# Optimization experiments

Hardware: AMD Instinct MI355X
Metric: run time of the kernel (lower is better)

Reference implementation:

```python
import jax, jax.numpy as jnp
import numpy as np

D = 1024
H = 16
DH = D // H
SCALE = DH ** -0.5
EPS = 1e-5


def setup_inputs() -> dict:
    key = jax.random.key(0)
    ks = jax.random.split(key, 8)
    B, K = 256, 64
    hidden = jax.random.normal(ks[0], (B, K, D), dtype=jnp.float32)
    active_mask = jax.random.bernoulli(ks[1], 0.5, (B, K))
    w = lambda k: jax.random.normal(k, (D, D), dtype=jnp.float32) * 0.02
    return {
        "hidden": hidden,
        "active_mask": active_mask,
        "W_q": w(ks[2]),
        "W_k": w(ks[3]),
        "W_v": w(ks[4]),
        "W_o": w(ks[5]),
        "ln_gamma": jnp.ones((D,), dtype=jnp.float32),
        "ln_beta": jnp.zeros((D,), dtype=jnp.float32),
    }


def reference(hidden, active_mask, W_q, W_k, W_v, W_o, ln_gamma, ln_beta):
    B, K, _ = hidden.shape
    # Linear (no bias): x @ W.T, then split heads -> [B, H, K, Dh]
    def heads(t):
        return t.reshape(B, K, H, DH).transpose(0, 2, 1, 3)
    Q = heads(hidden @ W_q.T)
    Km = heads(hidden @ W_k.T)
    V = heads(hidden @ W_v.T)
    # scaled dot-product scores [B, H, K, K]
    attn = jnp.einsum("bhqd,bhkd->bhqk", Q, Km) * SCALE
    attn = jax.nn.softmax(attn, axis=-1)
    # post-softmax row masking: inactive query rows get zero attention
    row_mask = active_mask[:, None, :, None].astype(attn.dtype)  # [B,1,K,1]
    attn = attn * row_mask
    out = jnp.einsum("bhqk,bhkd->bhqd", attn, V)
    out = out.transpose(0, 2, 1, 3).reshape(B, K, D)
    out = out @ W_o.T
    # gated residual: residual attention output only on active modules
    active_f = active_mask[:, :, None].astype(hidden.dtype)
    h_final = hidden + active_f * out
    # LayerNorm over last dim
    mu = jnp.mean(h_final, axis=-1, keepdims=True)
    var = jnp.var(h_final, axis=-1, keepdims=True)
    h_norm = (h_final - mu) * jax.lax.rsqrt(var + EPS)
    return h_norm * ln_gamma + ln_beta
```

## Files before the change

kernel.cpp:

```cpp
#include <hip/hip_runtime.h>
#include <hip/hip_bf16.h>
#include <stdint.h>

#define D_DIM 1024
#define NH 16
#define DHD 64
#define SEQ 64
#define NBATCH 256
#define M_TOT 16384
#define ATT_SCALE 0.125f
#define LN_EPS 1e-5f

#define BM 256
#define BN 256
#define BKT 64
#define NTK (D_DIM / BKT)

typedef __attribute__((ext_vector_type(8))) short bf16x8;
typedef __attribute__((ext_vector_type(4))) float f32x4;

__device__ __forceinline__ float bf2f(short s) {
  union { uint32_t u; float f; } c;
  c.u = ((uint32_t)(uint16_t)s) << 16;
  return c.f;
}

__device__ __forceinline__ short f2bf(float f) {
  union { __hip_bfloat16 h; short s; } c; c.h = __float2bfloat16(f);
  return c.s;
}

__device__ __forceinline__ bf16x8 cvt8(float4 a, float4 b) {
  bf16x8 r;
  r[0] = f2bf(a.x); r[1] = f2bf(a.y); r[2] = f2bf(a.z); r[3] = f2bf(a.w);
  r[4] = f2bf(b.x); r[5] = f2bf(b.y); r[6] = f2bf(b.z); r[7] = f2bf(b.w);
  return r;
}

__device__ __forceinline__ void cp16(const void* g, void* l) {
  __builtin_amdgcn_global_load_lds(
      (const __attribute__((address_space(1))) uint32_t*)g,
      (__attribute__((address_space(3))) uint32_t*)l, 16, 0, 0);
}

__global__ void conv_all(const float* __restrict__ Wq, const float* __restrict__ Wk,
                         const float* __restrict__ Wv, const float* __restrict__ Wo,
                         const float* __restrict__ H,
                         __hip_bfloat16* __restrict__ Wall,
                         __hip_bfloat16* __restrict__ Hb) {
  const size_t idx8 = ((size_t)blockIdx.x * 256 + threadIdx.x) * 8;
  const size_t WE = (size_t)4 * D_DIM * D_DIM;
  const float* src;
  __hip_bfloat16* dst;
  if (idx8 < WE) {
    int z = (int)(idx8 >> 20);
    size_t off = idx8 & ((1u << 20) - 1);
    src = ((z == 0) ? Wq : (z == 1) ? Wk : (z == 2) ? Wv : Wo) + off;
    dst = Wall + idx8;
  } else {
    size_t off = idx8 - WE;
    src = H + off;
    dst = Hb + off;
  }
  float4 a = ((const float4*)src)[0];
  float4 b = ((const float4*)src)[1];
  *(bf16x8*)(short*)dst = cvt8(a, b);
}

#define GEMM_TILE(J, CUR, NXT) do {                                           \
                 \
    _Pragma("unroll") for (int i_ = 0; i_ < 4; ++i_) {                        \
      af[i_][0] = *(const bf16x8*)(LdsA[CUR] + aoff + i_ * 2048 + colsw0);    \
      af[i_][1] = *(const bf16x8*)(LdsA[CUR] + aoff + i_ * 2048 + colsw1);    \
    }                                                                         \
    _Pragma("unroll") for (int q_ = 0; q_ < 2; ++q_) {                        \
      bfr[q_][0] = *(const bf16x8*)(LdsB[CUR] + boff + q_ * 2048 + colsw0);   \
      bfr[q_][1] = *(const bf16x8*)(LdsB[CUR] + boff + q_ * 2048 + colsw1);   \
    }                                                                         \
    __builtin_amdgcn_s_barrier();                                             \
    __asm volatile("s_waitcnt lgkmcnt(0)" ::: "memory");                      \
    __builtin_amdgcn_s_setprio(1);                                            \
    _Pragma("unroll") for (int i_ = 0; i_ < 4; ++i_)                          \
      _Pragma("unroll") for (int q_ = 0; q_ < 2; ++q_) {                      \
        acc[i_][q_] = __builtin_amdgcn_mfma_f32_16x16x32_bf16(                \
            af[i_][0], bfr[q_][0], acc[i_][q_], 0, 0, 0);                     \
        acc[i_][q_] = __builtin_amdgcn_mfma_f32_16x16x32_bf16(                \
            af[i_][1], bfr[q_][1], acc[i_][q_], 0, 0, 0);                     \
      }                                                                       \
    __builtin_amdgcn_s_setprio(0);                                            \
    __builtin_amdgcn_s_barrier();                                             \
           \
    _Pragma("unroll") for (int q_ = 0; q_ < 2; ++q_) {                        \
      bfr[2 + q_][0] =                                                        \
          *(const bf16x8*)(LdsB[CUR] + boff + (2 + q_) * 2048 + colsw0);      \
      bfr[2 + q_][1] =                                                        \
          *(const bf16x8*)(LdsB[CUR] + boff + (2 + q_) * 2048 + colsw1);      \
    }                                                                         \
    if ((J) + 2 < NTK) { STG_A(CUR, (J) + 2, 0); STG_A(CUR, (J) + 2, 2); }    \
    __builtin_amdgcn_s_barrier();                                             \
    __asm volatile("s_waitcnt lgkmcnt(0)" ::: "memory");                      \
    __builtin_amdgcn_s_setprio(1);                                            \
    _Pragma("unroll") for (int i_ = 0; i_ < 4; ++i_)                          \
      _Pragma("unroll") for (int q_ = 0; q_ < 2; ++q_) {                      \
        acc[i_][2 + q_] = __builtin_amdgcn_mfma_f32_16x16x32_bf16(            \
            af[i_][0], bfr[2 + q_][0], acc[i_][2 + q_], 0, 0, 0);             \
        acc[i_][2 + q_] = __builtin_amdgcn_mfma_f32_16x16x32_bf16(            \
            af[i_][1], bfr[2 + q_][1], acc[i_][2 + q_], 0, 0, 0);             \
      }                                                                       \
    __builtin_amdgcn_s_setprio(0);                                            \
    __builtin_amdgcn_s_barrier();                                             \
            \
    _Pragma("unroll") for (int i_ = 0; i_ < 4; ++i_) {                        \
      af[i_][0] =                                                             \
          *(const bf16x8*)(LdsA[CUR] + aoff + 8192 + i_ * 2048 + colsw0);     \
      af[i_][1] =                                                             \
          *(const bf16x8*)(LdsA[CUR] + aoff + 8192 + i_ * 2048 + colsw1);     \
    }                                                                         \
    if ((J) + 2 < NTK) {                                                      \
      STG_B(CUR, (J) + 2, 0); STG_B(CUR, (J) + 2, 1);                         \
      STG_B(CUR, (J) + 2, 2); STG_B(CUR, (J) + 2, 3);                         \
    }                                                                         \
    __builtin_amdgcn_s_barrier();                                             \
    __asm volatile("s_waitcnt lgkmcnt(0)" ::: "memory");                      \
    __builtin_amdgcn_s_setprio(1);                                            \
    _Pragma("unroll") for (int i_ = 0; i_ < 4; ++i_)                          \
      _Pragma("unroll") for (int q_ = 0; q_ < 2; ++q_) {                      \
        acc[4 + i_][2 + q_] = __builtin_amdgcn_mfma_f32_16x16x32_bf16(        \
            af[i_][0], bfr[2 + q_][0], acc[4 + i_][2 + q_], 0, 0, 0);         \
        acc[4 + i_][2 + q_] = __builtin_amdgcn_mfma_f32_16x16x32_bf16(        \
            af[i_][1], bfr[2 + q_][1], acc[4 + i_][2 + q_], 0, 0, 0);         \
      }                                                                       \
    __builtin_amdgcn_s_setprio(0);                                            \
    __builtin_amdgcn_s_barrier();                                             \
          \
    if ((J) + 2 < NTK) { STG_A(CUR, (J) + 2, 1); STG_A(CUR, (J) + 2, 3); }    \
    __builtin_amdgcn_s_setprio(1);                                            \
    _Pragma("unroll") for (int i_ = 0; i_ < 4; ++i_)                          \
      _Pragma("unroll") for (int q_ = 0; q_ < 2; ++q_) {                      \
        acc[4 + i_][q_] = __builtin_amdgcn_mfma_f32_16x16x32_bf16(            \
            af[i_][0], bfr[q_][0], acc[4 + i_][q_], 0, 0, 0);                 \
        acc[4 + i_][q_] = __builtin_amdgcn_mfma_f32_16x16x32_bf16(            \
            af[i_][1], bfr[q_][1], acc[4 + i_][q_], 0, 0, 0);                 \
      }                                                                       \
    __builtin_amdgcn_s_setprio(0);                                            \
    if ((J) + 2 < NTK) {                                                      \
      __asm volatile("s_waitcnt vmcnt(8)" ::: "memory");                      \
    } else if ((J) + 1 < NTK) {                                               \
      __asm volatile("s_waitcnt vmcnt(0)" ::: "memory");                      \
    }                                                                         \
    __builtin_amdgcn_s_barrier();                                             \
  } while (0)

#define GEMM_PIPELINE() do {                                                  \
                 \
    STG_A(0, 0, 0); STG_A(0, 0, 1); STG_A(0, 0, 2); STG_A(0, 0, 3);           \
    STG_B(0, 0, 0); STG_B(0, 0, 1); STG_B(0, 0, 2); STG_B(0, 0, 3);           \
    STG_A(1, 1, 0); STG_A(1, 1, 1); STG_A(1, 1, 2); STG_A(1, 1, 3);           \
    STG_B(1, 1, 0); STG_B(1, 1, 1); STG_B(1, 1, 2); STG_B(1, 1, 3);           \
    __asm volatile("s_waitcnt vmcnt(8)" ::: "memory");                        \
    __builtin_amdgcn_s_barrier();                                             \
    _Pragma("unroll 1") for (int it_ = 0; it_ < NTK / 2; ++it_) {             \
      GEMM_TILE(2 * it_, 0, 1);                                               \
      GEMM_TILE(2 * it_ + 1, 1, 0);                                           \
    }                                                                         \
  } while (0)

__global__ void __launch_bounds__(512, 2)
gemm_qkv_bf(const __hip_bfloat16* __restrict__ Hb,
            const __hip_bfloat16* __restrict__ Wall,
            __hip_bfloat16* __restrict__ Qw,
            __hip_bfloat16* __restrict__ Kw,
            __hip_bfloat16* __restrict__ Vtw) {
  __shared__ __align__(16) char LdsA[2][BM * BKT * 2];
  __shared__ __align__(16) char LdsB[2][BN * BKT * 2];
  const int tid = threadIdx.x;
  const int lane = tid & 63, wave = tid >> 6;
  const int l16 = lane & 15, kq = lane >> 4;
  const int wr = wave >> 2, wc = wave & 3;
  const int m0 = blockIdx.x * BM, n0 = blockIdx.y * BN;
  const __hip_bfloat16* Bm = Wall + (size_t)blockIdx.z * D_DIM * D_DIM;
  const int wub = wave * 1024;
  const int srow = tid >> 3;
  const int scol8 = (((tid >> 3) & 7) ^ (tid & 7)) << 3;
  const size_t a_thr = (size_t)(m0 + srow) * D_DIM + scol8;
  const size_t b_thr = (size_t)(n0 + srow) * D_DIM + scol8;
  const int colsw0 = (kq * 16) ^ ((l16 & 7) << 4);
  const int colsw1 = (64 + kq * 16) ^ ((l16 & 7) << 4);
  const int aoff = (wr * 128 + l16) * 128;
  const int boff = (wc * 64 + l16) * 128;

  f32x4 acc[8][4] = {};
  bf16x8 af[4][2], bfr[4][2];

#define STG_A(BUF, JT, Q)                                                      \
  cp16(Hb + a_thr + (size_t)(Q) * (64 * D_DIM) + (JT) * BKT,                   \
       LdsA[BUF] + (Q) * 8192 + wub)
#define STG_B(BUF, JT, Q)                                                      \
  cp16(Bm + b_thr + (size_t)(Q) * (64 * D_DIM) + (JT) * BKT,                   \
       LdsB[BUF] + (Q) * 8192 + wub)

  GEMM_PIPELINE();

#undef STG_A
#undef STG_B

  __hip_bfloat16* outp = (blockIdx.z == 0) ? Qw : (blockIdx.z == 1) ? Kw : Vtw;
  const int zlt2 = (blockIdx.z < 2);
#pragma unroll
  for (int i = 0; i < 8; ++i) {
#pragma unroll
    for (int r = 0; r < 4; ++r) {
      int gm = m0 + wr * 128 + i * 16 + kq * 4 + r;
      int b = gm >> 6, ks = gm & 63;
#pragma unroll
      for (int jf = 0; jf < 4; ++jf) {
        int gn = n0 + wc * 64 + jf * 16 + l16;
        int h = gn >> 6, dh = gn & 63;
        size_t idx = zlt2 ? ((size_t)(b * NH + h) * SEQ + ks) * DHD + dh
                          : ((size_t)(b * NH + h) * DHD + dh) * SEQ + ks;
        outp[idx] = __float2bfloat16(acc[i][jf][r]);
      }
    }
  }
}

__global__ void attn_v2(__hip_bfloat16* Qw,
                        const __hip_bfloat16* __restrict__ Kw,
                        const __hip_bfloat16* __restrict__ Vtw,
                        const int* __restrict__ mask) {
  __shared__ __align__(16) __hip_bfloat16 Ps[4][16 * 72];
  const int tid = threadIdx.x;
  const int lane = tid & 63;
  const int wave = tid >> 6;
  const int l16 = lane & 15, kq = lane >> 4;
  const int hh = blockIdx.x * 4 + wave;
  const int b = hh >> 4;
  const size_t base = (size_t)hh * 4096;
  __hip_bfloat16* Pw = &Ps[wave][0];

  bf16x8 kf[2][4], vf[2][4], qf[4][2];
#pragma unroll
  for (int kk2 = 0; kk2 < 2; ++kk2)
#pragma unroll
    for (int j = 0; j < 4; ++j) {
      kf[kk2][j] = *(const bf16x8*)(Kw + base + (j * 16 + l16) * 64 + kk2 * 32 + kq * 8);
      vf[kk2][j] = *(const bf16x8*)(Vtw + base + (j * 16 + l16) * 64 + kk2 * 32 + kq * 8);
    }
#pragma unroll
  for (int qt = 0; qt < 4; ++qt)
#pragma unroll
    for (int kk2 = 0; kk2 < 2; ++kk2)
      qf[qt][kk2] = *(const bf16x8*)(Qw + base + (qt * 16 + l16) * 64 + kk2 * 32 + kq * 8);

#pragma unroll
  for (int qt = 0; qt < 4; ++qt) {
    f32x4 accS[4] = {};
#pragma unroll
    for (int kk2 = 0; kk2 < 2; ++kk2)
#pragma unroll
      for (int j = 0; j < 4; ++j)
        accS[j] = __builtin_amdgcn_mfma_f32_16x16x32_bf16(qf[qt][kk2], kf[kk2][j],
                                                          accS[j], 0, 0, 0);
#pragma unroll
    for (int r = 0; r < 4; ++r) {
      float sv[4];
      float m = -1e30f;
#pragma unroll
      for (int j = 0; j < 4; ++j) { sv[j] = accS[j][r] * ATT_SCALE; m = fmaxf(m, sv[j]); }
#pragma unroll
      for (int off = 1; off < 16; off <<= 1) m = fmaxf(m, __shfl_xor(m, off, 64));
      float s = 0.f;
#pragma unroll
      for (int j = 0; j < 4; ++j) { sv[j] = __expf(sv[j] - m); s += sv[j]; }
#pragma unroll
      for (int off = 1; off < 16; off <<= 1) s += __shfl_xor(s, off, 64);
      float inv = 1.0f / s;
      int ql = kq * 4 + r;
#pragma unroll
      for (int j = 0; j < 4; ++j)
        Pw[ql * 72 + j * 16 + l16] = __float2bfloat16(sv[j] * inv);
    }
    __asm volatile("s_waitcnt lgkmcnt(0)" ::: "memory");

    f32x4 accO[4] = {};
#pragma unroll
    for (int kk2 = 0; kk2 < 2; ++kk2) {
      bf16x8 a = *(const bf16x8*)((const short*)Pw + l16 * 72 + kk2 * 32 + kq * 8);
#pragma unroll
      for (int j = 0; j < 4; ++j)
        accO[j] = __builtin_amdgcn_mfma_f32_16x16x32_bf16(a, vf[kk2][j], accO[j], 0, 0, 0);
    }
    __asm volatile("s_waitcnt lgkmcnt(0)" ::: "memory");

#pragma unroll
    for (int r = 0; r < 4; ++r) {
      int q = qt * 16 + kq * 4 + r;
      float mk = mask[b * SEQ + q] ? 1.0f : 0.0f;
#pragma unroll
      for (int j = 0; j < 4; ++j)
        Qw[base + q * DHD + j * 16 + l16] = __float2bfloat16(accO[j][r] * mk);
    }
  }
}

__global__ void __launch_bounds__(512, 2)
gemm_o(const __hip_bfloat16* __restrict__ Ow,
       const __hip_bfloat16* __restrict__ WoB,
       const int* __restrict__ mask,
       __hip_bfloat16* Hb) {
  __shared__ __align__(16) char LdsA[2][BM * BKT * 2];
  __shared__ __align__(16) char LdsB[2][BN * BKT * 2];
  const int tid = threadIdx.x;
  const int lane = tid & 63, wave = tid >> 6;
  const int l16 = lane & 15, kq = lane >> 4;
  const int wr = wave >> 2, wc = wave & 3;
  const int m0 = blockIdx.x * BM, n0 = blockIdx.y * BN;
  const int wub = wave * 1024;
  const int srow = tid >> 3;
  const int scol8 = (((tid >> 3) & 7) ^ (tid & 7)) << 3;
  const size_t ao_thr = ((size_t)(m0 >> 6) << 16) + (srow << 6) + scol8;
  const size_t b_thr = (size_t)(n0 + srow) * D_DIM + scol8;
  const int colsw0 = (kq * 16) ^ ((l16 & 7) << 4);
  const int colsw1 = (64 + kq * 16) ^ ((l16 & 7) << 4);
  const int aoff = (wr * 128 + l16) * 128;
  const int boff = (wc * 64 + l16) * 128;

  f32x4 acc[8][4] = {};
  bf16x8 af[4][2], bfr[4][2];

#define STG_A(BUF, JT, Q)                                                      \
  cp16(Ow + ao_thr + ((size_t)(Q) << 16) + ((size_t)(JT) << 12),               \
       LdsA[BUF] + (Q) * 8192 + wub)
#define STG_B(BUF, JT, Q)                                                      \
  cp16(WoB + b_thr + (size_t)(Q) * (64 * D_DIM) + (JT) * BKT,                  \
       LdsB[BUF] + (Q) * 8192 + wub)

  GEMM_PIPELINE();

#undef STG_A
#undef STG_B

#pragma unroll
  for (int i = 0; i < 8; ++i) {
#pragma unroll
    for (int r = 0; r < 4; ++r) {
      int gm = m0 + wr * 128 + i * 16 + kq * 4 + r;
      float mk = mask[gm] ? 1.0f : 0.0f;
#pragma unroll
      for (int jf = 0; jf < 4; ++jf) {
        int gn = n0 + wc * 64 + jf * 16 + l16;
        size_t idx = (size_t)gm * D_DIM + gn;
        Hb[idx] = __float2bfloat16(__bfloat162float(Hb[idx]) + mk * acc[i][jf][r]);
      }
    }
  }
}

__global__ void ln_bf(const __hip_bfloat16* __restrict__ Hf,
                      const float* __restrict__ gamma,
                      const float* __restrict__ beta,
                      float* __restrict__ out) {
  __shared__ float red[4];
  const int row = blockIdx.x, tid = threadIdx.x;
  const int wave = tid >> 6, lane = tid & 63;
  const size_t boff = (size_t)row * D_DIM + tid * 8;

  bf16x8 v = *(const bf16x8*)((const short*)Hf + boff);
  float f[8], s = 0.f, ss = 0.f;
#pragma unroll
  for (int k = 0; k < 8; ++k) { f[k] = bf2f(v[k]); s += f[k]; ss += f[k] * f[k]; }
#pragma unroll
  for (int off = 1; off < 64; off <<= 1) {
    s += __shfl_xor(s, off, 64);
    ss += __shfl_xor(ss, off, 64);
  }
  if (lane == 0) { red[wave * 2] = s; red[wave * 2 + 1] = ss; }
  __syncthreads();
  s = red[0] + red[2];
  ss = red[1] + red[3];
  const float mu = s * (1.0f / D_DIM);
  const float var = ss * (1.0f / D_DIM) - mu * mu;
  const float rs = rsqrtf(var + LN_EPS);

  float4 g0 = ((const float4*)(gamma + tid * 8))[0];
  float4 g1 = ((const float4*)(gamma + tid * 8))[1];
  float4 b0 = ((const float4*)(beta + tid * 8))[0];
  float4 b1 = ((const float4*)(beta + tid * 8))[1];
  float g[8] = {g0.x, g0.y, g0.z, g0.w, g1.x, g1.y, g1.z, g1.w};
  float bb[8] = {b0.x, b0.y, b0.z, b0.w, b1.x, b1.y, b1.z, b1.w};
  float o[8];
#pragma unroll
  for (int k = 0; k < 8; ++k)
    o[k] = (f[k] - mu) * rs * g[k] + bb[k];
  ((float4*)(out + boff))[0] = make_float4(o[0], o[1], o[2], o[3]);
  ((float4*)(out + boff))[1] = make_float4(o[4], o[5], o[6], o[7]);
}

extern "C" void kernel_launch(void* const* d_in, const int* in_sizes, int n_in,
                              void* d_out, int out_size, void* d_ws, size_t ws_size,
                              hipStream_t stream) {
  const float* hidden = (const float*)d_in[0];
  const int* mask = (const int*)d_in[1];
  const float* Wq = (const float*)d_in[2];
  const float* Wk = (const float*)d_in[3];
  const float* Wv = (const float*)d_in[4];
  const float* Wo = (const float*)d_in[5];
  const float* gamma = (const float*)d_in[6];
  const float* beta = (const float*)d_in[7];
  float* out = (float*)d_out;

  const size_t SZ = (size_t)M_TOT * D_DIM;
  __hip_bfloat16* Hb   = (__hip_bfloat16*)d_ws;
  __hip_bfloat16* Kw   = Hb + SZ;
  __hip_bfloat16* Qw   = Hb + 2 * SZ;
  __hip_bfloat16* Vtw  = Hb + 3 * SZ;
  __hip_bfloat16* Wall = Hb + 4 * SZ;

  conv_all<<<dim3(10240), 256, 0, stream>>>(Wq, Wk, Wv, Wo, hidden, Wall, Hb);
  gemm_qkv_bf<<<dim3(64, 4, 3), 512, 0, stream>>>(Hb, Wall, Qw, Kw, Vtw);
  attn_v2<<<dim3(1024), 256, 0, stream>>>(Qw, Kw, Vtw, mask);
  gemm_o<<<dim3(64, 4), 512, 0, stream>>>(Qw, Wall + 3 * D_DIM * D_DIM, mask, Hb);
  ln_bf<<<dim3(16384), 128, 0, stream>>>(Hb, gamma, beta, out);
}
```

Baseline: 336.7 us.

## Restructure GEMM tile loop with register double-buffered fragments and fewer barriers

Reorganizes the main GEMM k-loop used by both the QKV and output projections. All B fragments and the upper A fragments are now loaded up front into separate register sets. The next tile's lower A fragments are prefetched from the other LDS buffer while the last MFMA quadrant runs. The number of barriers and lgkmcnt waits per tile drops from about six to two, and all global-to-LDS staging is issued in one batch. The cost is higher VGPR pressure under the 512x2 launch bound and less interleaving of global loads with MFMA work.

```diff
diff --git a/kernel.cpp b/kernel.cpp
--- a/kernel.cpp
+++ b/kernel.cpp
@@ -68,97 +68,89 @@
 }
 
 #define GEMM_TILE(J, CUR, NXT) do {                                           \
-                 \
+                          \
+    _Pragma("unroll") for (int q_ = 0; q_ < 2; ++q_) {                        \
+      bl[q_][0] = *(const bf16x8*)(LdsB[CUR] + boff + q_ * 2048 + colsw0);    \
+      bl[q_][1] = *(const bf16x8*)(LdsB[CUR] + boff + q_ * 2048 + colsw1);    \
+    }                                                                         \
+    _Pragma("unroll") for (int q_ = 0; q_ < 2; ++q_) {                        \
+      bh[q_][0] =                                                             \
+          *(const bf16x8*)(LdsB[CUR] + boff + (2 + q_) * 2048 + colsw0);      \
+      bh[q_][1] =                                                             \
+          *(const bf16x8*)(LdsB[CUR] + boff + (2 + q_) * 2048 + colsw1);      \
+    }                                                                         \
     _Pragma("unroll") for (int i_ = 0; i_ < 4; ++i_) {                        \
-      af[i_][0] = *(const bf16x8*)(LdsA[CUR] + aoff + i_ * 2048 + colsw0);    \
-      af[i_][1] = *(const bf16x8*)(LdsA[CUR] + aoff + i_ * 2048 + colsw1);    \
-    }                                                                         \
-    _Pragma("unroll") for (int q_ = 0; q_ < 2; ++q_) {                        \
-      bfr[q_][0] = *(const bf16x8*)(LdsB[CUR] + boff + q_ * 2048 + colsw0);   \
-      bfr[q_][1] = *(const bf16x8*)(LdsB[CUR] + boff + q_ * 2048 + colsw1);   \
-    }                                                                         \
-    __builtin_amdgcn_s_barrier();                                             \
-    __asm volatile("s_waitcnt lgkmcnt(0)" ::: "memory");                      \
+      ah[i_][0] =                                                             \
+          *(const bf16x8*)(LdsA[CUR] + aoff + 8192 + i_ * 2048 + colsw0);     \
+      ah[i_][1] =                                                             \
+          *(const bf16x8*)(LdsA[CUR] + aoff + 8192 + i_ * 2048 + colsw1);     \
+    }                                                                         \
     __builtin_amdgcn_s_setprio(1);                                            \
     _Pragma("unroll") for (int i_ = 0; i_ < 4; ++i_)                          \
       _Pragma("unroll") for (int q_ = 0; q_ < 2; ++q_) {                      \
         acc[i_][q_] = __builtin_amdgcn_mfma_f32_16x16x32_bf16(                \
-            af[i_][0], bfr[q_][0], acc[i_][q_], 0, 0, 0);                     \
+            al[i_][0], bl[q_][0], acc[i_][q_], 0, 0, 0);                      \
         acc[i_][q_] = __builtin_amdgcn_mfma_f32_16x16x32_bf16(                \
-            af[i_][1], bfr[q_][1], acc[i_][q_], 0, 0, 0);                     \
+            al[i_][1], bl[q_][1], acc[i_][q_], 0, 0, 0);                      \
       }                                                                       \
-    __builtin_amdgcn_s_setprio(0);                                            \
-    __builtin_amdgcn_s_barrier();                                             \
-           \
-    _Pragma("unroll") for (int q_ = 0; q_ < 2; ++q_) {                        \
-      bfr[2 + q_][0] =                                                        \
-          *(const bf16x8*)(LdsB[CUR] + boff + (2 + q_) * 2048 + colsw0);      \
-      bfr[2 + q_][1] =                                                        \
-          *(const bf16x8*)(LdsB[CUR] + boff + (2 + q_) * 2048 + colsw1);      \
-    }                                                                         \
-    if ((J) + 2 < NTK) { STG_A(CUR, (J) + 2, 0); STG_A(CUR, (J) + 2, 2); }    \
-    __builtin_amdgcn_s_barrier();                                             \
-    __asm volatile("s_waitcnt lgkmcnt(0)" ::: "memory");                      \
-    __builtin_amdgcn_s_setprio(1);                                            \
     _Pragma("unroll") for (int i_ = 0; i_ < 4; ++i_)                          \
       _Pragma("unroll") for (int q_ = 0; q_ < 2; ++q_) {                      \
         acc[i_][2 + q_] = __builtin_amdgcn_mfma_f32_16x16x32_bf16(            \
-            af[i_][0], bfr[2 + q_][0], acc[i_][2 + q_], 0, 0, 0);             \
+            al[i_][0], bh[q_][0], acc[i_][2 + q_], 0, 0, 0);                  \
         acc[i_][2 + q_] = __builtin_amdgcn_mfma_f32_16x16x32_bf16(            \
-            af[i_][1], bfr[2 + q_][1], acc[i_][2 + q_], 0, 0, 0);             \
+            al[i_][1], bh[q_][1], acc[i_][2 + q_], 0, 0, 0);                  \
       }                                                                       \
-    __builtin_amdgcn_s_setprio(0);                                            \
-    __builtin_amdgcn_s_barrier();                                             \
-            \
-    _Pragma("unroll") for (int i_ = 0; i_ < 4; ++i_) {                        \
-      af[i_][0] =                                                             \
-          *(const bf16x8*)(LdsA[CUR] + aoff + 8192 + i_ * 2048 + colsw0);     \
-      af[i_][1] =                                                             \
-          *(const bf16x8*)(LdsA[CUR] + aoff + 8192 + i_ * 2048 + colsw1);     \
-    }                                                                         \
-    if ((J) + 2 < NTK) {                                                      \
-      STG_B(CUR, (J) + 2, 0); STG_B(CUR, (J) + 2, 1);                         \
-      STG_B(CUR, (J) + 2, 2); STG_B(CUR, (J) + 2, 3);                         \
-    }                                                                         \
-    __builtin_amdgcn_s_barrier();                                             \
-    __asm volatile("s_waitcnt lgkmcnt(0)" ::: "memory");                      \
-    __builtin_amdgcn_s_setprio(1);                                            \
     _Pragma("unroll") for (int i_ = 0; i_ < 4; ++i_)                          \
       _Pragma("unroll") for (int q_ = 0; q_ < 2; ++q_) {                      \
         acc[4 + i_][2 + q_] = __builtin_amdgcn_mfma_f32_16x16x32_bf16(        \
-            af[i_][0], bfr[2 + q_][0], acc[4 + i_][2 + q_], 0, 0, 0);         \
+            ah[i_][0], bh[q_][0], acc[4 + i_][2 + q_], 0, 0, 0);              \
         acc[4 + i_][2 + q_] = __builtin_amdgcn_mfma_f32_16x16x32_bf16(        \
-            af[i_][1], bfr[2 + q_][1], acc[4 + i_][2 + q_], 0, 0, 0);         \
+            ah[i_][1], bh[q_][1], acc[4 + i_][2 + q_], 0, 0, 0);              \
       }                                                                       \
     __builtin_amdgcn_s_setprio(0);                                            \
+    __asm volatile("s_waitcnt lgkmcnt(0)" ::: "memory");                      \
+    __builtin_amdgcn_sched_barrier(0);                                        \
     __builtin_amdgcn_s_barrier();                                             \
-          \
-    if ((J) + 2 < NTK) { STG_A(CUR, (J) + 2, 1); STG_A(CUR, (J) + 2, 3); }    \
+               \
+    if ((J) + 2 < NTK) {                                                      \
+      STG_A(CUR, (J) + 2, 0); STG_A(CUR, (J) + 2, 1);                         \
+      STG_A(CUR, (J) + 2, 2); STG_A(CUR, (J) + 2, 3);                         \
+      STG_B(CUR, (J) + 2, 0); STG_B(CUR, (J) + 2, 1);                         \
+      STG_B(CUR, (J) + 2, 2); STG_B(CUR, (J) + 2, 3);                         \
+      __asm volatile("s_waitcnt vmcnt(8)" ::: "memory");                      \
+    } else if ((J) + 1 < NTK) {                                               \
+      __asm volatile("s_waitcnt vmcnt(0)" ::: "memory");                      \
+    }                                                                         \
+    if ((J) + 1 < NTK) {                                                      \
+      __builtin_amdgcn_s_barrier();                                           \
+      _Pragma("unroll") for (int i_ = 0; i_ < 4; ++i_) {                      \
+        al[i_][0] = *(const bf16x8*)(LdsA[NXT] + aoff + i_ * 2048 + colsw0);  \
+        al[i_][1] = *(const bf16x8*)(LdsA[NXT] + aoff + i_ * 2048 + colsw1);  \
+      }                                                                       \
+    }                                                                         \
     __builtin_amdgcn_s_setprio(1);                                            \
     _Pragma("unroll") for (int i_ = 0; i_ < 4; ++i_)                          \
       _Pragma("unroll") for (int q_ = 0; q_ < 2; ++q_) {                      \
         acc[4 + i_][q_] = __builtin_amdgcn_mfma_f32_16x16x32_bf16(            \
-            af[i_][0], bfr[q_][0], acc[4 + i_][q_], 0, 0, 0);                 \
+            ah[i_][0], bl[q_][0], acc[4 + i_][q_], 0, 0, 0);                  \
         acc[4 + i_][q_] = __builtin_amdgcn_mfma_f32_16x16x32_bf16(            \
-            af[i_][1], bfr[q_][1], acc[4 + i_][q_], 0, 0, 0);                 \
+            ah[i_][1], bl[q_][1], acc[4 + i_][q_], 0, 0, 0);                  \
       }                                                                       \
     __builtin_amdgcn_s_setprio(0);                                            \
-    if ((J) + 2 < NTK) {                                                      \
-      __asm volatile("s_waitcnt vmcnt(8)" ::: "memory");                      \
-    } else if ((J) + 1 < NTK) {                                               \
-      __asm volatile("s_waitcnt vmcnt(0)" ::: "memory");                      \
-    }                                                                         \
-    __builtin_amdgcn_s_barrier();                                             \
   } while (0)
 
 #define GEMM_PIPELINE() do {                                                  \
-                 \
+         \
     STG_A(0, 0, 0); STG_A(0, 0, 1); STG_A(0, 0, 2); STG_A(0, 0, 3);           \
     STG_B(0, 0, 0); STG_B(0, 0, 1); STG_B(0, 0, 2); STG_B(0, 0, 3);           \
     STG_A(1, 1, 0); STG_A(1, 1, 1); STG_A(1, 1, 2); STG_A(1, 1, 3);           \
     STG_B(1, 1, 0); STG_B(1, 1, 1); STG_B(1, 1, 2); STG_B(1, 1, 3);           \
     __asm volatile("s_waitcnt vmcnt(8)" ::: "memory");                        \
     __builtin_amdgcn_s_barrier();                                             \
+    _Pragma("unroll") for (int i_ = 0; i_ < 4; ++i_) {                        \
+      al[i_][0] = *(const bf16x8*)(LdsA[0] + aoff + i_ * 2048 + colsw0);      \
+      al[i_][1] = *(const bf16x8*)(LdsA[0] + aoff + i_ * 2048 + colsw1);      \
+    }                                                                         \
     _Pragma("unroll 1") for (int it_ = 0; it_ < NTK / 2; ++it_) {             \
       GEMM_TILE(2 * it_, 0, 1);                                               \
       GEMM_TILE(2 * it_ + 1, 1, 0);                                           \
@@ -190,7 +182,7 @@
   const int boff = (wc * 64 + l16) * 128;
 
   f32x4 acc[8][4] = {};
-  bf16x8 af[4][2], bfr[4][2];
+  bf16x8 al[4][2], ah[4][2], bl[2][2], bh[2][2];
 
 #define STG_A(BUF, JT, Q)                                                      \
   cp16(Hb + a_thr + (size_t)(Q) * (64 * D_DIM) + (JT) * BKT,                   \
@@ -326,7 +318,7 @@
   const int boff = (wc * 64 + l16) * 128;
 
   f32x4 acc[8][4] = {};
-  bf16x8 af[4][2], bfr[4][2];
+  bf16x8 al[4][2], ah[4][2], bl[2][2], bh[2][2];
 
 #define STG_A(BUF, JT, Q)                                                      \
   cp16(Ow + ao_thr + ((size_t)(Q) << 16) + ((size_t)(JT) << 12),               \
```

Result: no change. 339.8 us (+0.9%).

## Fuse attention into output projection GEMM, computing per-head attention tiles in LDS

Applied to the files above, without the earlier changes.

Replaces the separate attention kernel and O-projection GEMM with one kernel. Each block covers two batches (128 rows) by 256 output columns and, for each K-tile (one head), computes that head's attention output into an LDS A-tile, then multiplies it with the staged Wo tile. This removes the write and re-read of the attention output through global memory and one launch. In exchange, attention is recomputed four times, once per column block (blockIdx.y), and the per-block M tile shrinks from 256 to 128 rows, lowering data reuse per block.

```diff
diff --git a/kernel.cpp b/kernel.cpp
--- a/kernel.cpp
+++ b/kernel.cpp
@@ -68,7 +68,6 @@
 }
 
 #define GEMM_TILE(J, CUR, NXT) do {                                           \
-                 \
     _Pragma("unroll") for (int i_ = 0; i_ < 4; ++i_) {                        \
       af[i_][0] = *(const bf16x8*)(LdsA[CUR] + aoff + i_ * 2048 + colsw0);    \
       af[i_][1] = *(const bf16x8*)(LdsA[CUR] + aoff + i_ * 2048 + colsw1);    \
@@ -89,7 +88,6 @@
       }                                                                       \
     __builtin_amdgcn_s_setprio(0);                                            \
     __builtin_amdgcn_s_barrier();                                             \
-           \
     _Pragma("unroll") for (int q_ = 0; q_ < 2; ++q_) {                        \
       bfr[2 + q_][0] =                                                        \
           *(const bf16x8*)(LdsB[CUR] + boff + (2 + q_) * 2048 + colsw0);      \
@@ -109,7 +107,6 @@
       }                                                                       \
     __builtin_amdgcn_s_setprio(0);                                            \
     __builtin_amdgcn_s_barrier();                                             \
-            \
     _Pragma("unroll") for (int i_ = 0; i_ < 4; ++i_) {                        \
       af[i_][0] =                                                             \
           *(const bf16x8*)(LdsA[CUR] + aoff + 8192 + i_ * 2048 + colsw0);     \
@@ -132,7 +129,6 @@
       }                                                                       \
     __builtin_amdgcn_s_setprio(0);                                            \
     __builtin_amdgcn_s_barrier();                                             \
-          \
     if ((J) + 2 < NTK) { STG_A(CUR, (J) + 2, 1); STG_A(CUR, (J) + 2, 3); }    \
     __builtin_amdgcn_s_setprio(1);                                            \
     _Pragma("unroll") for (int i_ = 0; i_ < 4; ++i_)                          \
@@ -152,7 +148,6 @@
   } while (0)
 
 #define GEMM_PIPELINE() do {                                                  \
-                 \
     STG_A(0, 0, 0); STG_A(0, 0, 1); STG_A(0, 0, 2); STG_A(0, 0, 3);           \
     STG_B(0, 0, 0); STG_B(0, 0, 1); STG_B(0, 0, 2); STG_B(0, 0, 3);           \
     STG_A(1, 1, 0); STG_A(1, 1, 1); STG_A(1, 1, 2); STG_A(1, 1, 3);           \
@@ -224,127 +219,142 @@
   }
 }
 
-__global__ void attn_v2(__hip_bfloat16* Qw,
-                        const __hip_bfloat16* __restrict__ Kw,
-                        const __hip_bfloat16* __restrict__ Vtw,
-                        const int* __restrict__ mask) {
-  __shared__ __align__(16) __hip_bfloat16 Ps[4][16 * 72];
-  const int tid = threadIdx.x;
-  const int lane = tid & 63;
-  const int wave = tid >> 6;
-  const int l16 = lane & 15, kq = lane >> 4;
-  const int hh = blockIdx.x * 4 + wave;
-  const int b = hh >> 4;
-  const size_t base = (size_t)hh * 4096;
-  __hip_bfloat16* Pw = &Ps[wave][0];
-
-  bf16x8 kf[2][4], vf[2][4], qf[4][2];
-#pragma unroll
-  for (int kk2 = 0; kk2 < 2; ++kk2)
-#pragma unroll
-    for (int j = 0; j < 4; ++j) {
-      kf[kk2][j] = *(const bf16x8*)(Kw + base + (j * 16 + l16) * 64 + kk2 * 32 + kq * 8);
-      vf[kk2][j] = *(const bf16x8*)(Vtw + base + (j * 16 + l16) * 64 + kk2 * 32 + kq * 8);
-    }
-#pragma unroll
-  for (int qt = 0; qt < 4; ++qt)
-#pragma unroll
-    for (int kk2 = 0; kk2 < 2; ++kk2)
-      qf[qt][kk2] = *(const bf16x8*)(Qw + base + (qt * 16 + l16) * 64 + kk2 * 32 + kq * 8);
-
-#pragma unroll
-  for (int qt = 0; qt < 4; ++qt) {
-    f32x4 accS[4] = {};
-#pragma unroll
-    for (int kk2 = 0; kk2 < 2; ++kk2)
-#pragma unroll
-      for (int j = 0; j < 4; ++j)
-        accS[j] = __builtin_amdgcn_mfma_f32_16x16x32_bf16(qf[qt][kk2], kf[kk2][j],
-                                                          accS[j], 0, 0, 0);
-#pragma unroll
-    for (int r = 0; r < 4; ++r) {
-      float sv[4];
-      float m = -1e30f;
-#pragma unroll
-      for (int j = 0; j < 4; ++j) { sv[j] = accS[j][r] * ATT_SCALE; m = fmaxf(m, sv[j]); }
-#pragma unroll
-      for (int off = 1; off < 16; off <<= 1) m = fmaxf(m, __shfl_xor(m, off, 64));
-      float s = 0.f;
-#pragma unroll
-      for (int j = 0; j < 4; ++j) { sv[j] = __expf(sv[j] - m); s += sv[j]; }
-#pragma unroll
-      for (int off = 1; off < 16; off <<= 1) s += __shfl_xor(s, off, 64);
-      float inv = 1.0f / s;
-      int ql = kq * 4 + r;
-#pragma unroll
-      for (int j = 0; j < 4; ++j)
-        Pw[ql * 72 + j * 16 + l16] = __float2bfloat16(sv[j] * inv);
-    }
-    __asm volatile("s_waitcnt lgkmcnt(0)" ::: "memory");
-
-    f32x4 accO[4] = {};
-#pragma unroll
-    for (int kk2 = 0; kk2 < 2; ++kk2) {
-      bf16x8 a = *(const bf16x8*)((const short*)Pw + l16 * 72 + kk2 * 32 + kq * 8);
-#pragma unroll
-      for (int j = 0; j < 4; ++j)
-        accO[j] = __builtin_amdgcn_mfma_f32_16x16x32_bf16(a, vf[kk2][j], accO[j], 0, 0, 0);
-    }
-    __asm volatile("s_waitcnt lgkmcnt(0)" ::: "memory");
-
-#pragma unroll
-    for (int r = 0; r < 4; ++r) {
-      int q = qt * 16 + kq * 4 + r;
-      float mk = mask[b * SEQ + q] ? 1.0f : 0.0f;
-#pragma unroll
-      for (int j = 0; j < 4; ++j)
-        Qw[base + q * DHD + j * 16 + l16] = __float2bfloat16(accO[j][r] * mk);
-    }
-  }
-}
-
 __global__ void __launch_bounds__(512, 2)
-gemm_o(const __hip_bfloat16* __restrict__ Ow,
-       const __hip_bfloat16* __restrict__ WoB,
-       const int* __restrict__ mask,
-       __hip_bfloat16* Hb) {
-  __shared__ __align__(16) char LdsA[2][BM * BKT * 2];
+attn_gemm_o(const __hip_bfloat16* __restrict__ Qw,
+            const __hip_bfloat16* __restrict__ Kw,
+            const __hip_bfloat16* __restrict__ Vtw,
+            const __hip_bfloat16* __restrict__ WoB,
+            const int* __restrict__ mask,
+            __hip_bfloat16* Hb) {
   __shared__ __align__(16) char LdsB[2][BN * BKT * 2];
+  __shared__ __align__(16) __hip_bfloat16 Atile[128 * 72];
+  __shared__ __align__(16) __hip_bfloat16 Ps[8][16 * 72];
   const int tid = threadIdx.x;
   const int lane = tid & 63, wave = tid >> 6;
   const int l16 = lane & 15, kq = lane >> 4;
   const int wr = wave >> 2, wc = wave & 3;
-  const int m0 = blockIdx.x * BM, n0 = blockIdx.y * BN;
-  const int wub = wave * 1024;
+  const int m0 = blockIdx.x * 128, n0 = blockIdx.y * BN;
+  const int b0 = blockIdx.x * 2;
   const int srow = tid >> 3;
   const int scol8 = (((tid >> 3) & 7) ^ (tid & 7)) << 3;
-  const size_t ao_thr = ((size_t)(m0 >> 6) << 16) + (srow << 6) + scol8;
   const size_t b_thr = (size_t)(n0 + srow) * D_DIM + scol8;
   const int colsw0 = (kq * 16) ^ ((l16 & 7) << 4);
   const int colsw1 = (64 + kq * 16) ^ ((l16 & 7) << 4);
-  const int aoff = (wr * 128 + l16) * 128;
   const int boff = (wc * 64 + l16) * 128;
-
-  f32x4 acc[8][4] = {};
-  bf16x8 af[4][2], bfr[4][2];
-
-#define STG_A(BUF, JT, Q)                                                      \
-  cp16(Ow + ao_thr + ((size_t)(Q) << 16) + ((size_t)(JT) << 12),               \
-       LdsA[BUF] + (Q) * 8192 + wub)
-#define STG_B(BUF, JT, Q)                                                      \
+  __hip_bfloat16* Pw = &Ps[wave][0];
+
+  f32x4 acc[4][4] = {};
+
+#define STG_OB(BUF, JT, Q)                                                     \
   cp16(WoB + b_thr + (size_t)(Q) * (64 * D_DIM) + (JT) * BKT,                  \
-       LdsB[BUF] + (Q) * 8192 + wub)
-
-  GEMM_PIPELINE();
-
-#undef STG_A
-#undef STG_B
-
-#pragma unroll
-  for (int i = 0; i < 8; ++i) {
+       LdsB[BUF] + (Q) * 8192 + wave * 1024)
+
+  STG_OB(0, 0, 0); STG_OB(0, 0, 1); STG_OB(0, 0, 2); STG_OB(0, 0, 3);
+  STG_OB(1, 1, 0); STG_OB(1, 1, 1); STG_OB(1, 1, 2); STG_OB(1, 1, 3);
+  __asm volatile("s_waitcnt vmcnt(4)" ::: "memory");
+  __builtin_amdgcn_s_barrier();
+
+#pragma unroll 1
+  for (int jt = 0; jt < NTK; ++jt) {
+    const int cur = jt & 1;
+    bf16x8 bfr[4][2];
+#pragma unroll
+    for (int q = 0; q < 4; ++q) {
+      bfr[q][0] = *(const bf16x8*)(LdsB[cur] + boff + q * 2048 + colsw0);
+      bfr[q][1] = *(const bf16x8*)(LdsB[cur] + boff + q * 2048 + colsw1);
+    }
+    const size_t hb = (((size_t)(b0 + wr) * NH) + jt) * 4096;
+    bf16x8 kf[2][4], vf[2][4], qf2[2];
+#pragma unroll
+    for (int kk2 = 0; kk2 < 2; ++kk2) {
+#pragma unroll
+      for (int j = 0; j < 4; ++j) {
+        kf[kk2][j] = *(const bf16x8*)(Kw + hb + (j * 16 + l16) * 64 + kk2 * 32 + kq * 8);
+        vf[kk2][j] = *(const bf16x8*)(Vtw + hb + (j * 16 + l16) * 64 + kk2 * 32 + kq * 8);
+      }
+      qf2[kk2] = *(const bf16x8*)(Qw + hb + (wc * 16 + l16) * 64 + kk2 * 32 + kq * 8);
+    }
+    f32x4 accS[4] = {};
+#pragma unroll
+    for (int kk2 = 0; kk2 < 2; ++kk2)
+#pragma unroll
+      for (int j = 0; j < 4; ++j)
+        accS[j] = __builtin_amdgcn_mfma_f32_16x16x32_bf16(qf2[kk2], kf[kk2][j],
+                                                          accS[j], 0, 0, 0);
 #pragma unroll
     for (int r = 0; r < 4; ++r) {
-      int gm = m0 + wr * 128 + i * 16 + kq * 4 + r;
+      float sv[4];
+      float m = -1e30f;
+#pragma unroll
+      for (int j = 0; j < 4; ++j) { sv[j] = accS[j][r] * ATT_SCALE; m = fmaxf(m, sv[j]); }
+#pragma unroll
+      for (int off = 1; off < 16; off <<= 1) m = fmaxf(m, __shfl_xor(m, off, 64));
+      float s = 0.f;
+#pragma unroll
+      for (int j = 0; j < 4; ++j) { sv[j] = __expf(sv[j] - m); s += sv[j]; }
+#pragma unroll
+      for (int off = 1; off < 16; off <<= 1) s += __shfl_xor(s, off, 64);
+      float inv = 1.0f / s;
+      int ql = kq * 4 + r;
+#pragma unroll
+      for (int j = 0; j < 4; ++j)
+        Pw[ql * 72 + j * 16 + l16] = __float2bfloat16(sv[j] * inv);
+    }
+    __asm volatile("s_waitcnt lgkmcnt(0)" ::: "memory");
+
+    f32x4 accO[4] = {};
+#pragma unroll
+    for (int kk2 = 0; kk2 < 2; ++kk2) {
+      bf16x8 a = *(const bf16x8*)((const short*)Pw + l16 * 72 + kk2 * 32 + kq * 8);
+#pragma unroll
+      for (int j = 0; j < 4; ++j)
+        accO[j] = __builtin_amdgcn_mfma_f32_16x16x32_bf16(a, vf[kk2][j], accO[j], 0, 0, 0);
+    }
+#pragma unroll
+    for (int r = 0; r < 4; ++r) {
+      int q = wc * 16 + kq * 4 + r;
+      float mk = mask[(b0 + wr) * SEQ + q] ? 1.0f : 0.0f;
+      int arow = wr * 64 + q;
+#pragma unroll
+      for (int j = 0; j < 4; ++j)
+        Atile[arow * 72 + j * 16 + l16] = __float2bfloat16(accO[j][r] * mk);
+    }
+    __asm volatile("s_waitcnt lgkmcnt(0)" ::: "memory");
+    __builtin_amdgcn_sched_barrier(0);
+    __builtin_amdgcn_s_barrier();
+    if (jt + 2 < NTK) {
+      STG_OB(cur, jt + 2, 0); STG_OB(cur, jt + 2, 1);
+      STG_OB(cur, jt + 2, 2); STG_OB(cur, jt + 2, 3);
+      __asm volatile("s_waitcnt vmcnt(4)" ::: "memory");
+    } else if (jt + 1 < NTK) {
+      __asm volatile("s_waitcnt vmcnt(0)" ::: "memory");
+    }
+    bf16x8 afr[4][2];
+#pragma unroll
+    for (int i = 0; i < 4; ++i) {
+      afr[i][0] = *(const bf16x8*)&Atile[(wr * 64 + i * 16 + l16) * 72 + kq * 8];
+      afr[i][1] = *(const bf16x8*)&Atile[(wr * 64 + i * 16 + l16) * 72 + 32 + kq * 8];
+    }
+    __builtin_amdgcn_s_setprio(1);
+#pragma unroll
+    for (int i = 0; i < 4; ++i)
+#pragma unroll
+      for (int q = 0; q < 4; ++q) {
+        acc[i][q] = __builtin_amdgcn_mfma_f32_16x16x32_bf16(
+            afr[i][0], bfr[q][0], acc[i][q], 0, 0, 0);
+        acc[i][q] = __builtin_amdgcn_mfma_f32_16x16x32_bf16(
+            afr[i][1], bfr[q][1], acc[i][q], 0, 0, 0);
+      }
+    __builtin_amdgcn_s_setprio(0);
+    __builtin_amdgcn_s_barrier();
+  }
+#undef STG_OB
+
+#pragma unroll
+  for (int i = 0; i < 4; ++i) {
+#pragma unroll
+    for (int r = 0; r < 4; ++r) {
+      int gm = m0 + wr * 64 + i * 16 + kq * 4 + r;
       float mk = mask[gm] ? 1.0f : 0.0f;
 #pragma unroll
       for (int jf = 0; jf < 4; ++jf) {
@@ -418,7 +428,8 @@
 
   conv_all<<<dim3(10240), 256, 0, stream>>>(Wq, Wk, Wv, Wo, hidden, Wall, Hb);
   gemm_qkv_bf<<<dim3(64, 4, 3), 512, 0, stream>>>(Hb, Wall, Qw, Kw, Vtw);
-  attn_v2<<<dim3(1024), 256, 0, stream>>>(Qw, Kw, Vtw, mask);
-  gemm_o<<<dim3(64, 4), 512, 0, stream>>>(Qw, Wall + 3 * D_DIM * D_DIM, mask, Hb);
+  attn_gemm_o<<<dim3(128, 4), 512, 0, stream>>>(Qw, Kw, Vtw,
+                                                Wall + (size_t)3 * D_DIM * D_DIM,
+                                                mask, Hb);
   ln_bf<<<dim3(16384), 128, 0, stream>>>(Hb, gamma, beta, out);
 }
```

Measured after the change: 457.0 us. 35.7% more time.
